# Kernel optimization log

Hardware: AMD Instinct MI355X
Metric: run time of the kernel (lower is better)

The kernel has to match this reference:

```python
import jax, jax.numpy as jnp
import numpy as np

DEPTH, B, H, E = 4, 4096, 1024, 1024  # embedDim == h so all layers stack


def setup_inputs() -> dict:
    key = jax.random.key(0)
    k1, k2, k3, k4 = jax.random.split(key, 4)
    x = jax.random.normal(k1, (B, E), dtype=jnp.float32)
    s_h = jax.random.normal(k2, (DEPTH, B, H), dtype=jnp.float32)
    s_c = jax.random.normal(k3, (DEPTH, B, H), dtype=jnp.float32)
    # Linear(embedDim + h, 4h) per layer; stored as [in, out] (transposed torch layout)
    W = jax.random.normal(k4, (DEPTH, E + H, 4 * H), dtype=jnp.float32) * 0.02
    b = jnp.zeros((DEPTH, 4 * H), dtype=jnp.float32)
    return {"x": x, "s_h": s_h, "s_c": s_c, "W": W, "b": b}


def _lstm_layer(out, layer_params):
    hh, c, Wl, bl = layer_params
    xh = jnp.concatenate([out, hh], axis=1)          # [B, E+H]
    z = xh @ Wl + bl                                  # [B, 4H]
    i, f, o, g = jnp.split(z, 4, axis=1)              # torch.split(Wx, h, 1) order: i,f,o,g
    i = jax.nn.sigmoid(i)
    f = jax.nn.sigmoid(f)
    o = jax.nn.sigmoid(o)
    g = jnp.tanh(g)
    # trainable=False -> no dropout on g
    c_new = c * f + g * i
    h_new = jnp.tanh(c_new) * o
    return h_new, (h_new, c_new)


def reference(x, s_h, s_c, W, b):
    # scan over depth: layer l consumes previous layer's output as its input
    out, (h_new, c_new) = jax.lax.scan(_lstm_layer, x, (s_h, s_c, W, b))
    return out, h_new, c_new
```

## Files before the change

kernel.cpp:

```cpp
#include <hip/hip_runtime.h>
#include <hip/hip_bf16.h>
#include <stdint.h>

#define DEPTH 4
#define Bb 4096
#define Hh 1024
#define Ee 1024
#define Kd 2048
#define Ng 4096

typedef __attribute__((ext_vector_type(8))) short short8;
typedef __attribute__((ext_vector_type(4))) float floatx4;
typedef __attribute__((ext_vector_type(4))) float f32x4;

__device__ __forceinline__ float fast_sigmoid(float x) {
  return 1.0f / (1.0f + __expf(-x));
}
__device__ __forceinline__ float fast_tanh(float x) {
  float t = __expf(-2.0f * fabsf(x));
  return copysignf((1.0f - t) / (1.0f + t), x);
}

__device__ __forceinline__ void gload_lds16(const void* g, void* l) {
  __builtin_amdgcn_global_load_lds(
      (const __attribute__((address_space(1))) void*)(uintptr_t)g,
      (__attribute__((address_space(3))) void*)(uint32_t)(uintptr_t)l,
      16, 0, 0);
}

__global__ __launch_bounds__(256) void transpose_w_kernel(
    const float* __restrict__ W, __hip_bfloat16* __restrict__ Wt) {
  __shared__ __attribute__((aligned(16))) float ldsT[64 * 132];
  const int l = blockIdx.z;
  const int k0 = blockIdx.x * 128;
  const int n0 = blockIdx.y * 64;
  const float* Wl = W + (size_t)l * Kd * Ng + (size_t)k0 * Ng + n0;
  __hip_bfloat16* Wtl = Wt + (size_t)l * Ng * Kd;
  const int tid = threadIdx.x;

#pragma unroll
  for (int i = 0; i < 8; i++) {
    const int flat = tid + 256 * i;
    const int k = flat >> 4;
    const int c4 = (flat & 15) * 4;
    const f32x4 v = *(const f32x4*)(Wl + (size_t)k * Ng + c4);
    const int grp = k >> 3;
    const int klo = k & 7;
#pragma unroll
    for (int j = 0; j < 4; j++) {
      const int n = c4 + j;
      ldsT[n * 132 + ((grp ^ ((n >> 2) & 3)) << 3) + klo] = v[j];
    }
  }
  __syncthreads();

#pragma unroll
  for (int i = 0; i < 4; i++) {
    const int c = tid + 256 * i;
    const int n = c >> 4;
    const int kc = c & 15;
    const int g = kc ^ ((n >> 2) & 3);
    const float* src = &ldsT[n * 132 + (g << 3)];
    const f32x4 u0 = *(const f32x4*)src;
    const f32x4 u1 = *(const f32x4*)(src + 4);
    union {
      __hip_bfloat16 h[8];
      short8 s;
    } p;
    p.h[0] = __float2bfloat16(u0.x);
    p.h[1] = __float2bfloat16(u0.y);
    p.h[2] = __float2bfloat16(u0.z);
    p.h[3] = __float2bfloat16(u0.w);
    p.h[4] = __float2bfloat16(u1.x);
    p.h[5] = __float2bfloat16(u1.y);
    p.h[6] = __float2bfloat16(u1.z);
    p.h[7] = __float2bfloat16(u1.w);
    *(short8*)&Wtl[(size_t)(n0 + n) * Kd + k0 + kc * 8] = p.s;
  }
}

__global__ __launch_bounds__(256) void prefill_xh_kernel(
    const float* __restrict__ x, const float* __restrict__ s_h,
    __hip_bfloat16* __restrict__ xh) {
  const int idx = blockIdx.x * blockDim.x + threadIdx.x;
  const int XN = Bb * Ee / 4;
  const int TOTAL = XN + DEPTH * Bb * Hh / 4;
  if (idx >= TOTAL) return;
  const float* srcp;
  __hip_bfloat16* dst;
  if (idx < XN) {
    const int b = idx >> 8;
    const int j4 = idx & 255;
    srcp = x + (size_t)idx * 4;
    dst = xh + (size_t)b * Kd + j4 * 4;
  } else {
    const int e4 = idx - XN;
    const int l = e4 >> 20;
    const int r = e4 & 0xFFFFF;
    const int b = r >> 8;
    const int j4 = r & 255;
    srcp = s_h + (size_t)e4 * 4;
    dst = xh + (size_t)l * Bb * Kd + (size_t)b * Kd + Ee + j4 * 4;
  }
  f32x4 v = *(const f32x4*)srcp;
  union {
    __hip_bfloat16 h[4];
    unsigned long long u;
  } p;
  p.h[0] = __float2bfloat16(v.x);
  p.h[1] = __float2bfloat16(v.y);
  p.h[2] = __float2bfloat16(v.z);
  p.h[3] = __float2bfloat16(v.w);
  *(unsigned long long*)dst = p.u;
}

__global__ __launch_bounds__(256, 4) void lstm_layer_kernel(
    const __hip_bfloat16* __restrict__ A, const __hip_bfloat16* __restrict__ Wt,
    const float* __restrict__ bias, const float* __restrict__ c_in,
    float* __restrict__ out_h, float* __restrict__ out_c,
    float* __restrict__ out_final, __hip_bfloat16* __restrict__ xh_next) {
  __shared__ __attribute__((aligned(16))) __hip_bfloat16 As[128 * 32];
  __shared__ __attribute__((aligned(16))) __hip_bfloat16 Bs[128 * 32];

  const int tid = threadIdx.x;
  const int lane = tid & 63;
  const int wave = tid >> 6;
  const int wm = wave >> 1;
  const int wn = wave & 1;
  const int m0 = blockIdx.y * 128;
  const int j0 = blockIdx.x * 32;

  const int s0 = tid, s1 = tid + 256;
  const int r0 = s0 >> 2, q0 = (s0 & 3) ^ ((r0 >> 1) & 3);
  const int r1 = s1 >> 2, q1 = (s1 & 3) ^ ((r1 >> 1) & 3);
  const __hip_bfloat16* a_src0 = A + (size_t)(m0 + r0) * Kd + q0 * 8;
  const __hip_bfloat16* a_src1 = A + (size_t)(m0 + r1) * Kd + q1 * 8;
  const int nb0 = (r0 >> 5) * Hh + j0 + (r0 & 31);
  const int nb1 = (r1 >> 5) * Hh + j0 + (r1 & 31);
  const __hip_bfloat16* b_src0 = Wt + (size_t)nb0 * Kd + q0 * 8;
  const __hip_bfloat16* b_src1 = Wt + (size_t)nb1 * Kd + q1 * 8;
  __hip_bfloat16* a_dst0 = As + s0 * 8;
  __hip_bfloat16* a_dst1 = As + s1 * 8;
  __hip_bfloat16* b_dst0 = Bs + s0 * 8;
  __hip_bfloat16* b_dst1 = Bs + s1 * 8;

  floatx4 acc[4][4];
#pragma unroll
  for (int mi = 0; mi < 4; mi++)
#pragma unroll
    for (int g = 0; g < 4; g++) acc[mi][g] = floatx4{0.f, 0.f, 0.f, 0.f};

  const int lm = lane & 15;
  const int qk = lane >> 4;

  int a_off[4], b_off[4];
#pragma unroll
  for (int mi = 0; mi < 4; mi++) {
    const int R = wm * 64 + mi * 16 + lm;
    a_off[mi] = (R * 4 + (qk ^ ((R >> 1) & 3))) * 8;
  }
#pragma unroll
  for (int g = 0; g < 4; g++) {
    const int T = g * 32 + wn * 16 + lm;
    b_off[g] = (T * 4 + (qk ^ ((T >> 1) & 3))) * 8;
  }

  for (int kt = 0; kt < Kd / 32; kt++) {
    const int koff = kt * 32;
    __syncthreads();
    gload_lds16(a_src0 + koff, a_dst0);
    gload_lds16(a_src1 + koff, a_dst1);
    gload_lds16(b_src0 + koff, b_dst0);
    gload_lds16(b_src1 + koff, b_dst1);
    __syncthreads();

    short8 afrag[4], bfrag[4];
#pragma unroll
    for (int mi = 0; mi < 4; mi++) afrag[mi] = *(const short8*)&As[a_off[mi]];
#pragma unroll
    for (int g = 0; g < 4; g++) bfrag[g] = *(const short8*)&Bs[b_off[g]];
#pragma unroll
    for (int mi = 0; mi < 4; mi++)
#pragma unroll
      for (int g = 0; g < 4; g++)
        acc[mi][g] = __builtin_amdgcn_mfma_f32_16x16x32_bf16(
            afrag[mi], bfrag[g], acc[mi][g], 0, 0, 0);
  }

  const int j = j0 + wn * 16 + lm;
  const float bi = bias[j];
  const float bf = bias[Hh + j];
  const float bo = bias[2 * Hh + j];
  const float bg = bias[3 * Hh + j];
#pragma unroll
  for (int mi = 0; mi < 4; mi++) {
    const int row0 = m0 + wm * 64 + mi * 16 + qk * 4;
#pragma unroll
    for (int r = 0; r < 4; r++) {
      const int row = row0 + r;
      const float zi = acc[mi][0][r] + bi;
      const float zf = acc[mi][1][r] + bf;
      const float zo = acc[mi][2][r] + bo;
      const float zg = acc[mi][3][r] + bg;
      const float ig = fast_sigmoid(zi);
      const float fg = fast_sigmoid(zf);
      const float og = fast_sigmoid(zo);
      const float gg = fast_tanh(zg);
      const float c = c_in[(size_t)row * Hh + j];
      const float cn = fmaf(c, fg, gg * ig);
      const float hn = fast_tanh(cn) * og;
      out_h[(size_t)row * Hh + j] = hn;
      out_c[(size_t)row * Hh + j] = cn;
      if (xh_next) xh_next[(size_t)row * Kd + j] = __float2bfloat16(hn);
      if (out_final) out_final[(size_t)row * Hh + j] = hn;
    }
  }
}

extern "C" void kernel_launch(void* const* d_in, const int* in_sizes, int n_in,
                              void* d_out, int out_size, void* d_ws,
                              size_t ws_size, hipStream_t stream) {
  const float* x = (const float*)d_in[0];
  const float* s_h = (const float*)d_in[1];
  const float* s_c = (const float*)d_in[2];
  const float* W = (const float*)d_in[3];
  const float* bias = (const float*)d_in[4];
  float* out = (float*)d_out;

  __hip_bfloat16* Wt = (__hip_bfloat16*)d_ws;
  __hip_bfloat16* xh =
      (__hip_bfloat16*)((char*)d_ws + (size_t)DEPTH * Ng * Kd * 2);

  transpose_w_kernel<<<dim3(Kd / 128, Ng / 64, DEPTH), 256, 0, stream>>>(W, Wt);
  prefill_xh_kernel<<<(Bb * Ee / 4 + DEPTH * Bb * Hh / 4) / 256, 256, 0,
                      stream>>>(x, s_h, xh);

  float* out_h = out + (size_t)Bb * Ee;
  float* out_c = out_h + (size_t)DEPTH * Bb * Hh;
  for (int l = 0; l < DEPTH; l++) {
    lstm_layer_kernel<<<dim3(Hh / 32, Bb / 128), 256, 0, stream>>>(
        xh + (size_t)l * Bb * Kd, Wt + (size_t)l * Ng * Kd,
        bias + (size_t)l * Ng, s_c + (size_t)l * Bb * Hh,
        out_h + (size_t)l * Bb * Hh, out_c + (size_t)l * Bb * Hh,
        (l == DEPTH - 1) ? out : nullptr,
        (l < DEPTH - 1) ? xh + (size_t)(l + 1) * Bb * Kd : nullptr);
  }
}
```

Before: 754.9 us.

## Use 256x256 tiles with double-buffered async LDS loads interleaved with MFMA

```diff
diff --git a/kernel.cpp b/kernel.cpp
--- a/kernel.cpp
+++ b/kernel.cpp
@@ -8,6 +8,7 @@
 #define Ee 1024
 #define Kd 2048
 #define Ng 4096
+#define NT (Kd / 64)
 
 typedef __attribute__((ext_vector_type(8))) short short8;
 typedef __attribute__((ext_vector_type(4))) float floatx4;
@@ -114,92 +115,155 @@
   *(unsigned long long*)dst = p.u;
 }
 
-__global__ __launch_bounds__(256, 4) void lstm_layer_kernel(
+__global__ __launch_bounds__(512, 2) void lstm_layer_kernel(
     const __hip_bfloat16* __restrict__ A, const __hip_bfloat16* __restrict__ Wt,
     const float* __restrict__ bias, const float* __restrict__ c_in,
     float* __restrict__ out_h, float* __restrict__ out_c,
     float* __restrict__ out_final, __hip_bfloat16* __restrict__ xh_next) {
-  __shared__ __attribute__((aligned(16))) __hip_bfloat16 As[128 * 32];
-  __shared__ __attribute__((aligned(16))) __hip_bfloat16 Bs[128 * 32];
+  __shared__ __attribute__((aligned(16))) __hip_bfloat16 sm[4 * 256 * 64];
 
   const int tid = threadIdx.x;
   const int lane = tid & 63;
   const int wave = tid >> 6;
-  const int wm = wave >> 1;
-  const int wn = wave & 1;
-  const int m0 = blockIdx.y * 128;
-  const int j0 = blockIdx.x * 32;
-
-  const int s0 = tid, s1 = tid + 256;
-  const int r0 = s0 >> 2, q0 = (s0 & 3) ^ ((r0 >> 1) & 3);
-  const int r1 = s1 >> 2, q1 = (s1 & 3) ^ ((r1 >> 1) & 3);
-  const __hip_bfloat16* a_src0 = A + (size_t)(m0 + r0) * Kd + q0 * 8;
-  const __hip_bfloat16* a_src1 = A + (size_t)(m0 + r1) * Kd + q1 * 8;
-  const int nb0 = (r0 >> 5) * Hh + j0 + (r0 & 31);
-  const int nb1 = (r1 >> 5) * Hh + j0 + (r1 & 31);
-  const __hip_bfloat16* b_src0 = Wt + (size_t)nb0 * Kd + q0 * 8;
-  const __hip_bfloat16* b_src1 = Wt + (size_t)nb1 * Kd + q1 * 8;
-  __hip_bfloat16* a_dst0 = As + s0 * 8;
-  __hip_bfloat16* a_dst1 = As + s1 * 8;
-  __hip_bfloat16* b_dst0 = Bs + s0 * 8;
-  __hip_bfloat16* b_dst1 = Bs + s1 * 8;
-
-  floatx4 acc[4][4];
-#pragma unroll
-  for (int mi = 0; mi < 4; mi++)
+  const int wm = wave >> 2;
+  const int wn = wave & 3;
+  const int m0 = blockIdx.y * 256;
+  const int j0 = blockIdx.x * 64;
+
+  const int r0 = tid >> 3;
+  const int p = tid & 7;
+  const int q = p ^ (r0 & 7);
+  const __hip_bfloat16* aSrc[2][2];
+  const __hip_bfloat16* bSrc[2][2];
+#pragma unroll
+  for (int h = 0; h < 2; h++)
+#pragma unroll
+    for (int i = 0; i < 2; i++) {
+      const int r = r0 + i * 64;
+      const int ar = m0 + h * 128 + r;
+      aSrc[h][i] = A + (size_t)ar * Kd + q * 8;
+      const int tr = h * 128 + r;
+      const int nrow = (tr >> 6) * Hh + j0 + (tr & 63);
+      bSrc[h][i] = Wt + (size_t)nrow * Kd + q * 8;
+    }
+
+#define STAGEA(h, kt, buf)                                                  \
+  do {                                                                      \
+    __hip_bfloat16* _d = sm + (buf) * 16384 + (h) * 8192 + tid * 8;         \
+    gload_lds16(aSrc[h][0] + (kt) * 64, _d);                                \
+    gload_lds16(aSrc[h][1] + (kt) * 64, _d + 4096);                         \
+  } while (0)
+#define STAGEB(h, kt, buf)                                                  \
+  do {                                                                      \
+    __hip_bfloat16* _d = sm + 32768 + (buf) * 16384 + (h) * 8192 + tid * 8; \
+    gload_lds16(bSrc[h][0] + (kt) * 64, _d);                                \
+    gload_lds16(bSrc[h][1] + (kt) * 64, _d + 4096);                         \
+  } while (0)
+
+  const int qk = lane >> 4;
+  const int lm = lane & 15;
+  const int pc0 = qk ^ (lm & 7);
+  const int pc1 = (4 + qk) ^ (lm & 7);
+  const int aBase = (wm * 128 + lm) * 64;
+  const int bBase = (wn * 16 + lm) * 64;
+
+  floatx4 acc[8][4];
+#pragma unroll
+  for (int mi = 0; mi < 8; mi++)
 #pragma unroll
     for (int g = 0; g < 4; g++) acc[mi][g] = floatx4{0.f, 0.f, 0.f, 0.f};
 
-  const int lm = lane & 15;
-  const int qk = lane >> 4;
-
-  int a_off[4], b_off[4];
-#pragma unroll
-  for (int mi = 0; mi < 4; mi++) {
-    const int R = wm * 64 + mi * 16 + lm;
-    a_off[mi] = (R * 4 + (qk ^ ((R >> 1) & 3))) * 8;
-  }
-#pragma unroll
-  for (int g = 0; g < 4; g++) {
-    const int T = g * 32 + wn * 16 + lm;
-    b_off[g] = (T * 4 + (qk ^ ((T >> 1) & 3))) * 8;
-  }
-
-  for (int kt = 0; kt < Kd / 32; kt++) {
-    const int koff = kt * 32;
-    __syncthreads();
-    gload_lds16(a_src0 + koff, a_dst0);
-    gload_lds16(a_src1 + koff, a_dst1);
-    gload_lds16(b_src0 + koff, b_dst0);
-    gload_lds16(b_src1 + koff, b_dst1);
-    __syncthreads();
-
-    short8 afrag[4], bfrag[4];
-#pragma unroll
-    for (int mi = 0; mi < 4; mi++) afrag[mi] = *(const short8*)&As[a_off[mi]];
-#pragma unroll
-    for (int g = 0; g < 4; g++) bfrag[g] = *(const short8*)&Bs[b_off[g]];
-#pragma unroll
-    for (int mi = 0; mi < 4; mi++)
-#pragma unroll
-      for (int g = 0; g < 4; g++)
+  STAGEA(0, 0, 0);
+  STAGEA(1, 0, 0);
+  STAGEB(0, 0, 0);
+  STAGEB(1, 0, 0);
+  STAGEA(0, 1, 1);
+  STAGEA(1, 1, 1);
+  STAGEB(0, 1, 1);
+  asm volatile("s_waitcnt vmcnt(6)" ::: "memory");
+  __builtin_amdgcn_sched_barrier(0);
+  __builtin_amdgcn_s_barrier();
+
+  for (int t = 0; t < NT; ++t) {
+    const int cur = t & 1;
+    const __hip_bfloat16* As_c = sm + cur * 16384;
+    const __hip_bfloat16* Bs_c = sm + 32768 + cur * 16384;
+
+    short8 af[8][2];
+    short8 bfg[2];
+
+#pragma unroll
+    for (int mi = 0; mi < 8; mi++) {
+      af[mi][0] = *(const short8*)&As_c[aBase + mi * 1024 + pc0 * 8];
+      af[mi][1] = *(const short8*)&As_c[aBase + mi * 1024 + pc1 * 8];
+    }
+    bfg[0] = *(const short8*)&Bs_c[bBase + pc0 * 8];
+    bfg[1] = *(const short8*)&Bs_c[bBase + pc1 * 8];
+    if (t + 1 < NT) STAGEB(1, t + 1, cur ^ 1);
+    __builtin_amdgcn_s_barrier();
+    asm volatile("s_waitcnt lgkmcnt(0)" ::: "memory");
+    __builtin_amdgcn_sched_barrier(0);
+    __builtin_amdgcn_s_setprio(1);
+#pragma unroll
+    for (int mi = 0; mi < 8; mi++) {
+      acc[mi][0] = __builtin_amdgcn_mfma_f32_16x16x32_bf16(af[mi][0], bfg[0],
+                                                           acc[mi][0], 0, 0, 0);
+      acc[mi][0] = __builtin_amdgcn_mfma_f32_16x16x32_bf16(af[mi][1], bfg[1],
+                                                           acc[mi][0], 0, 0, 0);
+    }
+    __builtin_amdgcn_s_setprio(0);
+    __builtin_amdgcn_s_barrier();
+
+#pragma unroll
+    for (int g = 1; g < 4; g++) {
+      bfg[0] = *(const short8*)&Bs_c[bBase + g * 4096 + pc0 * 8];
+      bfg[1] = *(const short8*)&Bs_c[bBase + g * 4096 + pc1 * 8];
+      if (t + 2 < NT) {
+        if (g == 1)
+          STAGEA(0, t + 2, cur);
+        else if (g == 2)
+          STAGEA(1, t + 2, cur);
+        else
+          STAGEB(0, t + 2, cur);
+      }
+      __builtin_amdgcn_s_barrier();
+      asm volatile("s_waitcnt lgkmcnt(0)" ::: "memory");
+      __builtin_amdgcn_sched_barrier(0);
+      __builtin_amdgcn_s_setprio(1);
+#pragma unroll
+      for (int mi = 0; mi < 8; mi++) {
         acc[mi][g] = __builtin_amdgcn_mfma_f32_16x16x32_bf16(
-            afrag[mi], bfrag[g], acc[mi][g], 0, 0, 0);
+            af[mi][0], bfg[0], acc[mi][g], 0, 0, 0);
+        acc[mi][g] = __builtin_amdgcn_mfma_f32_16x16x32_bf16(
+            af[mi][1], bfg[1], acc[mi][g], 0, 0, 0);
+      }
+      __builtin_amdgcn_s_setprio(0);
+      if (g < 3) {
+        __builtin_amdgcn_s_barrier();
+      } else {
+        if (t < NT - 2)
+          asm volatile("s_waitcnt vmcnt(6)" ::: "memory");
+        else
+          asm volatile("s_waitcnt vmcnt(0)" ::: "memory");
+        __builtin_amdgcn_sched_barrier(0);
+        __builtin_amdgcn_s_barrier();
+      }
+    }
   }
 
   const int j = j0 + wn * 16 + lm;
   const float bi = bias[j];
-  const float bf = bias[Hh + j];
+  const float bf_ = bias[Hh + j];
   const float bo = bias[2 * Hh + j];
   const float bg = bias[3 * Hh + j];
 #pragma unroll
-  for (int mi = 0; mi < 4; mi++) {
-    const int row0 = m0 + wm * 64 + mi * 16 + qk * 4;
+  for (int mi = 0; mi < 8; mi++) {
+    const int row0 = m0 + wm * 128 + mi * 16 + qk * 4;
 #pragma unroll
     for (int r = 0; r < 4; r++) {
       const int row = row0 + r;
       const float zi = acc[mi][0][r] + bi;
-      const float zf = acc[mi][1][r] + bf;
+      const float zf = acc[mi][1][r] + bf_;
       const float zo = acc[mi][2][r] + bo;
       const float zg = acc[mi][3][r] + bg;
       const float ig = fast_sigmoid(zi);
@@ -215,6 +279,8 @@
       if (out_final) out_final[(size_t)row * Hh + j] = hn;
     }
   }
+#undef STAGEA
+#undef STAGEB
 }
 
 extern "C" void kernel_launch(void* const* d_in, const int* in_sizes, int n_in,
@@ -238,7 +304,7 @@
   float* out_h = out + (size_t)Bb * Ee;
   float* out_c = out_h + (size_t)DEPTH * Bb * Hh;
   for (int l = 0; l < DEPTH; l++) {
-    lstm_layer_kernel<<<dim3(Hh / 32, Bb / 128), 256, 0, stream>>>(
+    lstm_layer_kernel<<<dim3(Hh / 64, Bb / 256), 512, 0, stream>>>(
         xh + (size_t)l * Bb * Kd, Wt + (size_t)l * Ng * Kd,
         bias + (size_t)l * Ng, s_c + (size_t)l * Bb * Hh,
         out_h + (size_t)l * Bb * Hh, out_c + (size_t)l * Bb * Hh,
```

New measurement: 660.6 us. -12.5%, faster.
